# Performance work log

Hardware: AMD Instinct MI355X
Metric: run time of the kernel (lower is better)

Reference implementation:

```python
import jax, jax.numpy as jnp
import numpy as np

L, N, D, E, KD = 4, 40000, 128, 320000, 16
DECAY, N_ITER, EPS = 0.5, 3, 1e-5


def setup_inputs() -> dict:
    key = jax.random.key(0)
    ks = jax.random.split(key, 16)
    s = 0.05
    return {
        "x": jax.random.normal(ks[0], (L, N, D), jnp.float32),
        "edge_rows": jax.random.randint(ks[1], (E,), 0, N, jnp.int32),
        "edge_cols": jax.random.randint(ks[2], (E,), 0, N, jnp.int32),
        "edge_vals": jax.random.uniform(ks[3], (E,), jnp.float32) * 0.1,
        "sage_W": jax.random.normal(ks[4], (D, D), jnp.float32) * s,
        "sage_b": jnp.zeros((D,), jnp.float32),
        "sage_agg_W": jax.random.normal(ks[5], (D, D), jnp.float32) * s,
        "key_W": jax.random.normal(ks[6], (D, KD), jnp.float32) * s,
        "query_W": jax.random.normal(ks[7], (D, KD), jnp.float32) * s,
        "value_W": jax.random.normal(ks[8], (D, D), jnp.float32) * s,
        "attn_ln_g": jnp.ones((D,), jnp.float32),
        "attn_ln_b": jnp.zeros((D,), jnp.float32),
        "lin_W": jax.random.normal(ks[9], (D, D), jnp.float32) * s,
        "lin_b": jnp.zeros((D,), jnp.float32),
        "ln_g": jnp.ones((D,), jnp.float32),
        "ln_b": jnp.zeros((D,), jnp.float32),
    }


def _layernorm(x, g, b):
    mu = jnp.mean(x, axis=-1, keepdims=True)
    var = jnp.mean((x - mu) ** 2, axis=-1, keepdims=True)
    return (x - mu) * jax.lax.rsqrt(var + EPS) * g + b


def _spmm(rows, cols, vals, x2d):
    # sparse [N,N] @ dense [N,F]: out[r] = sum_e vals[e] * x2d[cols[e]] for rows[e]==r
    return jax.ops.segment_sum(vals[:, None] * x2d[cols], rows, num_segments=N)


def reference(x, edge_rows, edge_cols, edge_vals, sage_W, sage_b, sage_agg_W,
              key_W, query_W, value_W, attn_ln_g, attn_ln_b,
              lin_W, lin_b, ln_g, ln_b):
    # x: [L, N, D]
    x2d = jnp.transpose(x, (1, 0, 2)).reshape(N, L * D)  # [N, L*D]

    # ---- SAGEConv ----
    proj = x @ sage_W + sage_b
    agg = _spmm(edge_rows, edge_cols, edge_vals, x2d)
    agg = jnp.transpose(agg.reshape(N, L, D), (1, 0, 2)) @ sage_agg_W
    sage_out = jax.nn.silu(proj + agg)

    # ---- RetentiveAttention ----
    weights = jnp.mean((x @ key_W) * (x @ query_W), axis=-1, keepdims=True)
    x_acc = x
    cur = x2d
    for _ in range(1, N_ITER):
        cur = _spmm(edge_rows, edge_cols, edge_vals, cur * DECAY)
        xr = jnp.transpose(cur.reshape(N, L, D), (1, 0, 2))  # [L, N, D]
        weights = weights + jnp.mean((xr @ key_W) * (xr @ query_W), axis=-1, keepdims=True)
        x_acc = x_acc + xr
    attn_out = _layernorm((x_acc @ value_W) * weights, attn_ln_g, attn_ln_b)

    # ---- GPSConv fusion ----
    y = jax.nn.silu((sage_out + attn_out) @ lin_W + lin_b)
    return _layernorm(y, ln_g, ln_b)
```

## Files before the change

kernel.cpp:

```cpp
#include <hip/hip_runtime.h>
#include <math.h>

#define LL 4
#define NN 40000
#define DD 128
#define EE 320000
#define ROWS (LL*NN)
#define ND (NN*DD)
#define EPS_LN 1e-5f

typedef __attribute__((ext_vector_type(8))) short bf16x8;
typedef __attribute__((ext_vector_type(4))) short s16x4;
typedef __attribute__((ext_vector_type(4))) float f32x4;

#define OFF_CNT      0
#define OFF_ROWPTR   40000
#define OFF_ROWOFS   80004
#define OFF_CCOLS    120004
#define OFF_CVALS    440004
#define OFF_WBF      760004
#define OFF_A        829636
#define OFF_B        (OFF_A + ROWS*DD/2)
#define OFF_XBF      (OFF_B + ROWS*DD/2)

#define WB_W0  0
#define WB_W1  32768
#define WB_WV  65536
#define WB_WL  98304
#define WB_K   131072
#define WB_Q   135168
#define WB_LO_BIG 16384
#define WB_LO_KQ  2048
#define WB_LOGICAL 69632

__device__ __forceinline__ unsigned fu(float f) { union { float f; unsigned u; } v; v.f = f; return v.u; }
__device__ __forceinline__ float uf(unsigned u) { union { unsigned u; float f; } v; v.u = u; return v.f; }

__device__ __forceinline__ short f2bf(float f) {
    unsigned u = fu(f);
    unsigned r = u + 0x7fffu + ((u >> 16) & 1u);
    return (short)(r >> 16);
}
__device__ __forceinline__ float bf2f(short h) { return uf(((unsigned)(unsigned short)h) << 16); }
__device__ __forceinline__ void splitbf(float v, short& h, short& l) {
    h = f2bf(v);
    l = f2bf(v - bf2f(h));
}

__device__ __forceinline__ unsigned pack_hi(float a, float b) {
    return (fu(a) >> 16) | (fu(b) & 0xffff0000u);
}
__device__ __forceinline__ float resid(float a) {
    return a - uf(fu(a) & 0xffff0000u);
}

union FragU { bf16x8 v; unsigned u[4]; };

__global__ void k_hist(const int* __restrict__ rows, int* __restrict__ cnt) {
    int e = blockIdx.x * 256 + threadIdx.x;
    if (e < EE) atomicAdd(&cnt[rows[e]], 1);
}

__global__ __launch_bounds__(1024) void k_scan1(const int* __restrict__ cnt,
                                                int* __restrict__ row_ptr,
                                                int* __restrict__ bsum) {
    __shared__ int wtot[16];
    int tid = threadIdx.x, lane = tid & 63, wid = tid >> 6;
    int i = blockIdx.x * 1024 + tid;
    int v = (i < NN) ? cnt[i] : 0;
    int incl = v;
    #pragma unroll
    for (int off = 1; off < 64; off <<= 1) {
        int t = __shfl_up(incl, off);
        if (lane >= off) incl += t;
    }
    if (lane == 63) wtot[wid] = incl;
    __syncthreads();
    if (wid == 0) {
        int wv = (lane < 16) ? wtot[lane] : 0;
        #pragma unroll
        for (int off = 1; off < 16; off <<= 1) {
            int t = __shfl_up(wv, off);
            if (lane >= off) wv += t;
        }
        if (lane < 16) wtot[lane] = wv;
    }
    __syncthreads();
    int excl = ((wid > 0) ? wtot[wid - 1] : 0) + incl - v;
    if (i < NN) row_ptr[i] = excl;
    if (tid == 0) bsum[blockIdx.x] = wtot[15];
}

__global__ void k_scan2(const int* __restrict__ bsum, int* __restrict__ bofs) {
    int lane = threadIdx.x;
    int v = (lane < 40) ? bsum[lane] : 0;
    int incl = v;
    #pragma unroll
    for (int off = 1; off < 64; off <<= 1) {
        int t = __shfl_up(incl, off);
        if (lane >= off) incl += t;
    }
    if (lane < 40) bofs[lane] = incl - v;
    if (lane == 39) bofs[40] = incl;
}

__global__ __launch_bounds__(1024) void k_scan3(const int* __restrict__ bofs,
                                                int* __restrict__ row_ptr,
                                                int* __restrict__ row_ofs) {
    int i = blockIdx.x * 1024 + threadIdx.x;
    int add = bofs[blockIdx.x];
    if (i < NN) {
        int v = row_ptr[i] + add;
        row_ptr[i] = v;
        row_ofs[i] = v;
    }
    if (i == NN) row_ptr[NN] = bofs[40];
}

__global__ void k_scatter(const int* __restrict__ rows, const int* __restrict__ cols,
                          const float* __restrict__ vals, int* __restrict__ row_ofs,
                          int* __restrict__ csr_cols, float* __restrict__ csr_vals) {
    int e = blockIdx.x * 256 + threadIdx.x;
    if (e < EE) {
        int r = rows[e];
        int p = atomicAdd(&row_ofs[r], 1);
        csr_cols[p] = cols[e];
        csr_vals[p] = vals[e];
    }
}

__global__ __launch_bounds__(256) void k_xcast(const float* __restrict__ x, short* __restrict__ o) {
    size_t i = ((size_t)blockIdx.x * 256 + threadIdx.x) * 8;
    f32x4 a = *(const f32x4*)(x + i);
    f32x4 b = *(const f32x4*)(x + i + 4);
    bf16x8 r;
    #pragma unroll
    for (int j = 0; j < 4; ++j) { r[j] = f2bf(a[j]); r[j + 4] = f2bf(b[j]); }
    *(bf16x8*)(o + i) = r;
}

__global__ __launch_bounds__(64) void k_spmm(const short* __restrict__ in,
                                             const int* __restrict__ row_ptr,
                                             const int* __restrict__ ccols,
                                             const float* __restrict__ cvals,
                                             short* __restrict__ out) {
    int r = blockIdx.x;
    int lane = threadIdx.x;
    int l = lane >> 4;
    int c8 = (lane & 15) * 8;
    const short* inl = in + (size_t)l * ND + c8;
    float acc[8] = {0.f, 0.f, 0.f, 0.f, 0.f, 0.f, 0.f, 0.f};
    int e0 = row_ptr[r], e1 = row_ptr[r + 1];
    int e = e0;
    for (; e + 8 <= e1; e += 8) {
        int cc[8]; float vv[8]; bf16x8 xv[8];
        #pragma unroll
        for (int j = 0; j < 8; ++j) { cc[j] = ccols[e + j]; vv[j] = cvals[e + j]; }
        #pragma unroll
        for (int j = 0; j < 8; ++j) xv[j] = *(const bf16x8*)(inl + (size_t)cc[j] * DD);
        #pragma unroll
        for (int j = 0; j < 8; ++j)
            #pragma unroll
            for (int k = 0; k < 8; ++k) acc[k] += vv[j] * bf2f(xv[j][k]);
    }
    for (; e + 4 <= e1; e += 4) {
        int cc[4]; float vv[4]; bf16x8 xv[4];
        #pragma unroll
        for (int j = 0; j < 4; ++j) { cc[j] = ccols[e + j]; vv[j] = cvals[e + j]; }
        #pragma unroll
        for (int j = 0; j < 4; ++j) xv[j] = *(const bf16x8*)(inl + (size_t)cc[j] * DD);
        #pragma unroll
        for (int j = 0; j < 4; ++j)
            #pragma unroll
            for (int k = 0; k < 8; ++k) acc[k] += vv[j] * bf2f(xv[j][k]);
    }
    for (; e < e1; ++e) {
        int c = ccols[e];
        float v = cvals[e];
        bf16x8 xv = *(const bf16x8*)(inl + (size_t)c * DD);
        #pragma unroll
        for (int k = 0; k < 8; ++k) acc[k] += v * bf2f(xv[k]);
    }
    bf16x8 o;
    #pragma unroll
    for (int k = 0; k < 8; ++k) o[k] = f2bf(acc[k]);
    *(bf16x8*)(out + (size_t)l * ND + (size_t)r * DD + c8) = o;
}

__global__ void k_prep(const float* __restrict__ W0, const float* __restrict__ W1,
                       const float* __restrict__ Wv, const float* __restrict__ Wl,
                       const float* __restrict__ Kw, const float* __restrict__ Qw,
                       short* __restrict__ o) {
    int t = blockIdx.x * 256 + threadIdx.x;
    if (t >= WB_LOGICAL) return;
    float v;
    int hi_idx, lo_idx;
    if (t < 65536) {
        int m = t >> 14, idx = t & 16383;
        int nn = idx >> 7, kk = idx & 127;
        const float* M = (m == 0) ? W0 : (m == 1) ? W1 : (m == 2) ? Wv : Wl;
        v = M[kk * 128 + nn];
        hi_idx = m * 32768 + idx;
        lo_idx = hi_idx + WB_LO_BIG;
    } else {
        int t2 = t - 65536;
        int sel = t2 >> 11;
        int idx = t2 & 2047;
        int nn = idx >> 7, kk = idx & 127;
        const float* M = sel ? Qw : Kw;
        v = M[kk * 16 + nn];
        hi_idx = WB_K + sel * 4096 + idx;
        lo_idx = hi_idx + WB_LO_KQ;
    }
    short h, l;
    splitbf(v, h, l);
    o[hi_idx] = h;
    o[lo_idx] = l;
}

#define MFMA(a, b, c) __builtin_amdgcn_mfma_f32_16x16x32_bf16(a, b, c, 0, 0, 0)

__global__ __launch_bounds__(256, 4) void k_dense(
    const float* __restrict__ x, const short* __restrict__ A, const short* __restrict__ B,
    const short* __restrict__ wbf,
    const float* __restrict__ sage_b, const float* __restrict__ attn_g,
    const float* __restrict__ attn_b, const float* __restrict__ lin_b,
    const float* __restrict__ ln_g, const float* __restrict__ ln_b,
    float* __restrict__ out)
{
    __shared__ short pv[4][2][2048];
    const int tid = threadIdx.x;
    const int w = tid >> 6;
    const int lane = tid & 63;
    const int n = lane & 15;
    const int q = lane >> 4;
    const size_t rowA = (size_t)blockIdx.x * 64 + w * 16 + n;
    char* pB = (char*)&pv[w][0][0];
    char* vB = (char*)&pv[w][1][0];

    bf16x8 xh[4], ah[4], ch[4];
    f32x4 kx = {0,0,0,0}, qx = {0,0,0,0};
    f32x4 ka = {0,0,0,0}, qa = {0,0,0,0};
    f32x4 kb = {0,0,0,0}, qb = {0,0,0,0};

    {
        const float* xp = x + rowA * 128 + q * 8;
        const short* ap = A + rowA * 128 + q * 8;
        const short* bp = B + rowA * 128 + q * 8;
        const short* Kp = wbf + WB_K + n * 128 + q * 8;
        const short* Qp = wbf + WB_Q + n * 128 + q * 8;
        #pragma unroll
        for (int s = 0; s < 4; ++s) {
            f32x4 x0 = *(const f32x4*)(xp + s * 32);
            f32x4 x1 = *(const f32x4*)(xp + s * 32 + 4);
            bf16x8 av = *(const bf16x8*)(ap + s * 32);
            bf16x8 bv = *(const bf16x8*)(bp + s * 32);

            f32x4 c0, c1;
            #pragma unroll
            for (int j = 0; j < 4; ++j) {
                c0[j] = x0[j] + 0.5f * bf2f(av[j])     + 0.25f * bf2f(bv[j]);
                c1[j] = x1[j] + 0.5f * bf2f(av[j + 4]) + 0.25f * bf2f(bv[j + 4]);
            }

            FragU fxh, fxl, fch;
            #pragma unroll
            for (int i = 0; i < 2; ++i) {
                fxh.u[i]     = pack_hi(x0[2*i], x0[2*i+1]);
                fxh.u[i + 2] = pack_hi(x1[2*i], x1[2*i+1]);
                fxl.u[i]     = pack_hi(resid(x0[2*i]), resid(x0[2*i+1]));
                fxl.u[i + 2] = pack_hi(resid(x1[2*i]), resid(x1[2*i+1]));
                fch.u[i]     = pack_hi(c0[2*i], c0[2*i+1]);
                fch.u[i + 2] = pack_hi(c1[2*i], c1[2*i+1]);
            }
            xh[s] = fxh.v; ah[s] = av; ch[s] = fch.v;

            bf16x8 bkh = *(const bf16x8*)(Kp + s * 32);
            bf16x8 bkl = *(const bf16x8*)(Kp + WB_LO_KQ + s * 32);
            bf16x8 bqh = *(const bf16x8*)(Qp + s * 32);
            bf16x8 bql = *(const bf16x8*)(Qp + WB_LO_KQ + s * 32);
            kx = MFMA(fxh.v, bkh, kx); kx = MFMA(fxl.v, bkh, kx); kx = MFMA(fxh.v, bkl, kx);
            qx = MFMA(fxh.v, bqh, qx); qx = MFMA(fxl.v, bqh, qx); qx = MFMA(fxh.v, bql, qx);
            ka = MFMA(av, bkh, ka); qa = MFMA(av, bqh, qa);
            kb = MFMA(bv, bkh, kb); qb = MFMA(bv, bqh, qb);
        }
    }

    f32x4 wts;
    #pragma unroll
    for (int r = 0; r < 4; ++r) {
        float p = kx[r] * qx[r] + 0.25f * (ka[r] * qa[r]) + 0.0625f * (kb[r] * qb[r]);
        p += __shfl_xor(p, 1);
        p += __shfl_xor(p, 2);
        p += __shfl_xor(p, 4);
        p += __shfl_xor(p, 8);
        wts[r] = p * (1.f / 16.f);
    }

    {
        f32x4 S[8];
        #pragma unroll
        for (int t = 0; t < 8; ++t) {
            float bv = sage_b[t * 16 + n];
            S[t] = (f32x4){bv, bv, bv, bv};
        }
        #pragma unroll
        for (int s = 0; s < 4; ++s) {
            #pragma unroll
            for (int t = 0; t < 8; ++t) {
                bf16x8 w0h = *(const bf16x8*)(wbf + WB_W0 + (t * 16 + n) * 128 + s * 32 + q * 8);
                S[t] = MFMA(xh[s], w0h, S[t]);
                bf16x8 w1h = *(const bf16x8*)(wbf + WB_W1 + (t * 16 + n) * 128 + s * 32 + q * 8);
                S[t] = MFMA(ah[s], w1h, S[t]);
            }
        }
        #pragma unroll
        for (int t = 0; t < 8; ++t)
            #pragma unroll
            for (int r = 0; r < 4; ++r) {
                float v = S[t][r];
                v = v / (1.f + __expf(-v));
                int row = q * 4 + r;
                int byte = (row * 256 + (t * 16 + n) * 2) ^ ((row & 7) << 4);
                *(short*)(pB + byte) = f2bf(v);
            }
    }

    float mu_n, rs_n;
    {
        f32x4 V[8];
        #pragma unroll
        for (int t = 0; t < 8; ++t) V[t] = (f32x4){0.f, 0.f, 0.f, 0.f};
        #pragma unroll
        for (int s = 0; s < 4; ++s)
            #pragma unroll
            for (int t = 0; t < 8; ++t) {
                bf16x8 wvh = *(const bf16x8*)(wbf + WB_WV + (t * 16 + n) * 128 + s * 32 + q * 8);
                V[t] = MFMA(ch[s], wvh, V[t]);
            }
        f32x4 s1 = {0,0,0,0}, s2 = {0,0,0,0};
        #pragma unroll
        for (int t = 0; t < 8; ++t)
            #pragma unroll
            for (int r = 0; r < 4; ++r) {
                float v = V[t][r] * wts[r];
                V[t][r] = v;
                s1[r] += v; s2[r] += v * v;
            }
        #pragma unroll
        for (int r = 0; r < 4; ++r) {
            float a1 = s1[r], a2 = s2[r];
            a1 += __shfl_xor(a1, 1); a2 += __shfl_xor(a2, 1);
            a1 += __shfl_xor(a1, 2); a2 += __shfl_xor(a2, 2);
            a1 += __shfl_xor(a1, 4); a2 += __shfl_xor(a2, 4);
            a1 += __shfl_xor(a1, 8); a2 += __shfl_xor(a2, 8);
            s1[r] = a1; s2[r] = a2;
        }
        float mu4[4], rs4[4];
        #pragma unroll
        for (int r = 0; r < 4; ++r) {
            mu4[r] = s1[r] * (1.f / 128.f);
            float var = s2[r] * (1.f / 128.f) - mu4[r] * mu4[r];
            rs4[r] = rsqrtf(var + EPS_LN);
        }
        #pragma unroll
        for (int t = 0; t < 8; ++t)
            #pragma unroll
            for (int r = 0; r < 4; ++r) {
                int row = q * 4 + r;
                int byte = (row * 256 + (t * 16 + n) * 2) ^ ((row & 7) << 4);
                *(short*)(vB + byte) = f2bf(V[t][r]);
            }
        int src = (n >> 2) << 4;
        float mA = __shfl(mu4[0], src), mB_ = __shfl(mu4[1], src);
        float mC = __shfl(mu4[2], src), mD = __shfl(mu4[3], src);
        float rA = __shfl(rs4[0], src), rB_ = __shfl(rs4[1], src);
        float rC = __shfl(rs4[2], src), rD = __shfl(rs4[3], src);
        float m01 = (n & 1) ? mB_ : mA, m23 = (n & 1) ? mD : mC;
        float r01 = (n & 1) ? rB_ : rA, r23 = (n & 1) ? rD : rC;
        mu_n = (n & 2) ? m23 : m01;
        rs_n = (n & 2) ? r23 : r01;
    }

    bf16x8 zh[4];
    #pragma unroll
    for (int s = 0; s < 4; ++s) {
        int byte = (n * 256 + s * 64 + q * 16) ^ ((n & 7) << 4);
        bf16x8 ph = *(const bf16x8*)(pB + byte);
        bf16x8 vh = *(const bf16x8*)(vB + byte);
        const float* gp = attn_g + s * 32 + q * 8;
        const float* bp = attn_b + s * 32 + q * 8;
        f32x4 g0 = *(const f32x4*)gp, g1 = *(const f32x4*)(gp + 4);
        f32x4 b0 = *(const f32x4*)bp, b1 = *(const f32x4*)(bp + 4);
        float z[8];
        #pragma unroll
        for (int j = 0; j < 4; ++j) {
            z[j]     = bf2f(ph[j])     + (bf2f(vh[j])     - mu_n) * rs_n * g0[j] + b0[j];
            z[j + 4] = bf2f(ph[j + 4]) + (bf2f(vh[j + 4]) - mu_n) * rs_n * g1[j] + b1[j];
        }
        FragU f;
        f.u[0] = pack_hi(z[0], z[1]); f.u[1] = pack_hi(z[2], z[3]);
        f.u[2] = pack_hi(z[4], z[5]); f.u[3] = pack_hi(z[6], z[7]);
        zh[s] = f.v;
    }
    f32x4 F[8];
    #pragma unroll
    for (int t = 0; t < 8; ++t) {
        float bv = lin_b[t * 16 + n];
        F[t] = (f32x4){bv, bv, bv, bv};
    }
    #pragma unroll
    for (int s = 0; s < 4; ++s)
        #pragma unroll
        for (int t = 0; t < 8; ++t) {
            bf16x8 wlh = *(const bf16x8*)(wbf + WB_WL + (t * 16 + n) * 128 + s * 32 + q * 8);
            F[t] = MFMA(zh[s], wlh, F[t]);
        }
    f32x4 t1 = {0,0,0,0}, t2 = {0,0,0,0};
    #pragma unroll
    for (int t = 0; t < 8; ++t)
        #pragma unroll
        for (int r = 0; r < 4; ++r) {
            float v = F[t][r];
            v = v / (1.f + __expf(-v));
            F[t][r] = v;
            t1[r] += v; t2[r] += v * v;
        }
    #pragma unroll
    for (int r = 0; r < 4; ++r) {
        float a1 = t1[r], a2 = t2[r];
        a1 += __shfl_xor(a1, 1); a2 += __shfl_xor(a2, 1);
        a1 += __shfl_xor(a1, 2); a2 += __shfl_xor(a2, 2);
        a1 += __shfl_xor(a1, 4); a2 += __shfl_xor(a2, 4);
        a1 += __shfl_xor(a1, 8); a2 += __shfl_xor(a2, 8);
        t1[r] = a1; t2[r] = a2;
    }
    #pragma unroll
    for (int t = 0; t < 8; ++t) {
        float g = ln_g[t * 16 + n];
        float bb = ln_b[t * 16 + n];
        #pragma unroll
        for (int r = 0; r < 4; ++r) {
            float mu = t1[r] * (1.f / 128.f);
            float var = t2[r] * (1.f / 128.f) - mu * mu;
            float rs = rsqrtf(var + EPS_LN);
            size_t row = (size_t)blockIdx.x * 64 + w * 16 + q * 4 + r;
            out[row * 128 + t * 16 + n] = (F[t][r] - mu) * rs * g + bb;
        }
    }
}

extern "C" void kernel_launch(void* const* d_in, const int* in_sizes, int n_in,
                              void* d_out, int out_size, void* d_ws, size_t ws_size,
                              hipStream_t stream) {
    const float* x       = (const float*)d_in[0];
    const int*   erows   = (const int*)d_in[1];
    const int*   ecols   = (const int*)d_in[2];
    const float* evals   = (const float*)d_in[3];
    const float* sage_W  = (const float*)d_in[4];
    const float* sage_b  = (const float*)d_in[5];
    const float* sage_aW = (const float*)d_in[6];
    const float* key_W   = (const float*)d_in[7];
    const float* query_W = (const float*)d_in[8];
    const float* value_W = (const float*)d_in[9];
    const float* attn_g  = (const float*)d_in[10];
    const float* attn_b  = (const float*)d_in[11];
    const float* lin_W   = (const float*)d_in[12];
    const float* lin_b   = (const float*)d_in[13];
    const float* ln_g    = (const float*)d_in[14];
    const float* ln_b    = (const float*)d_in[15];
    float* out = (float*)d_out;

    int*   wsi = (int*)d_ws;
    float* wsf = (float*)d_ws;
    int*   cnt      = wsi + OFF_CNT;
    int*   row_ptr  = wsi + OFF_ROWPTR;
    int*   row_ofs  = wsi + OFF_ROWOFS;
    int*   csr_cols = wsi + OFF_CCOLS;
    float* csr_vals = wsf + OFF_CVALS;
    short* wbf      = (short*)(wsf + OFF_WBF);
    short* Abf      = (short*)(wsf + OFF_A);
    short* Bbf      = (short*)(wsf + OFF_B);
    short* Xbf      = (short*)(wsf + OFF_XBF);
    int*   bsum     = (int*)(wsf + OFF_A);
    int*   bofs     = bsum + 64;

    hipMemsetAsync(cnt, 0, NN * sizeof(int), stream);
    k_hist<<<(EE + 255) / 256, 256, 0, stream>>>(erows, cnt);
    k_prep<<<(WB_LOGICAL + 255) / 256, 256, 0, stream>>>(sage_W, sage_aW, value_W, lin_W,
                                                         key_W, query_W, wbf);
    k_xcast<<<ROWS * DD / (256 * 8), 256, 0, stream>>>(x, Xbf);
    k_scan1<<<40, 1024, 0, stream>>>(cnt, row_ptr, bsum);
    k_scan2<<<1, 64, 0, stream>>>(bsum, bofs);
    k_scan3<<<40, 1024, 0, stream>>>(bofs, row_ptr, row_ofs);
    k_scatter<<<(EE + 255) / 256, 256, 0, stream>>>(erows, ecols, evals, row_ofs, csr_cols, csr_vals);

    k_spmm<<<NN, 64, 0, stream>>>(Xbf, row_ptr, csr_cols, csr_vals, Abf);
    k_spmm<<<NN, 64, 0, stream>>>(Abf, row_ptr, csr_cols, csr_vals, Bbf);

    k_dense<<<ROWS / 64, 256, 0, stream>>>(x, Abf, Bbf, wbf, sage_b, attn_g, attn_b,
                                           lin_b, ln_g, ln_b, out);
}
```

Baseline: 597.8 us.

## Store bf16 node features node-major to gather contiguous rows in SpMM

Changes the bf16 feature buffers from [L,N,D] to a node-major [N,L*D] layout. Each SpMM gather then reads one contiguous 1KB row per edge instead of four 256B pieces, and SpMM blocks now hold four rows of 64 threads each. The dense kernel indexes the new layout and moves the combined-input fragments into LDS to cut register pressure, dropping the occupancy hint in launch_bounds. Fewer blocks and the wider gathers aim to improve memory efficiency, at the cost of extra LDS traffic in the dense kernel.

```diff
diff --git a/kernel.cpp b/kernel.cpp
--- a/kernel.cpp
+++ b/kernel.cpp
@@ -130,25 +130,29 @@
 }
 
 __global__ __launch_bounds__(256) void k_xcast(const float* __restrict__ x, short* __restrict__ o) {
-    size_t i = ((size_t)blockIdx.x * 256 + threadIdx.x) * 8;
-    f32x4 a = *(const f32x4*)(x + i);
-    f32x4 b = *(const f32x4*)(x + i + 4);
-    bf16x8 r;
-    #pragma unroll
-    for (int j = 0; j < 4; ++j) { r[j] = f2bf(a[j]); r[j + 4] = f2bf(b[j]); }
-    *(bf16x8*)(o + i) = r;
-}
-
-__global__ __launch_bounds__(64) void k_spmm(const short* __restrict__ in,
-                                             const int* __restrict__ row_ptr,
-                                             const int* __restrict__ ccols,
-                                             const float* __restrict__ cvals,
-                                             short* __restrict__ out) {
-    int r = blockIdx.x;
-    int lane = threadIdx.x;
-    int l = lane >> 4;
-    int c8 = (lane & 15) * 8;
-    const short* inl = in + (size_t)l * ND + c8;
+    int t = blockIdx.x * 256 + threadIdx.x;
+    int n = t >> 4;
+    int d8 = (t & 15) * 8;
+    #pragma unroll
+    for (int l = 0; l < LL; ++l) {
+        const float* xp = x + (size_t)l * ND + (size_t)n * 128 + d8;
+        f32x4 a = *(const f32x4*)xp;
+        f32x4 b = *(const f32x4*)(xp + 4);
+        bf16x8 r;
+        #pragma unroll
+        for (int j = 0; j < 4; ++j) { r[j] = f2bf(a[j]); r[j + 4] = f2bf(b[j]); }
+        *(bf16x8*)(o + (size_t)n * 512 + l * 128 + d8) = r;
+    }
+}
+
+__global__ __launch_bounds__(256) void k_spmm(const short* __restrict__ in,
+                                              const int* __restrict__ row_ptr,
+                                              const int* __restrict__ ccols,
+                                              const float* __restrict__ cvals,
+                                              short* __restrict__ out) {
+    int r = blockIdx.x * 4 + (threadIdx.x >> 6);
+    int lane = threadIdx.x & 63;
+    const short* inl = in + lane * 8;
     float acc[8] = {0.f, 0.f, 0.f, 0.f, 0.f, 0.f, 0.f, 0.f};
     int e0 = row_ptr[r], e1 = row_ptr[r + 1];
     int e = e0;
@@ -157,7 +161,7 @@
         #pragma unroll
         for (int j = 0; j < 8; ++j) { cc[j] = ccols[e + j]; vv[j] = cvals[e + j]; }
         #pragma unroll
-        for (int j = 0; j < 8; ++j) xv[j] = *(const bf16x8*)(inl + (size_t)cc[j] * DD);
+        for (int j = 0; j < 8; ++j) xv[j] = *(const bf16x8*)(inl + (size_t)cc[j] * 512);
         #pragma unroll
         for (int j = 0; j < 8; ++j)
             #pragma unroll
@@ -168,7 +172,7 @@
         #pragma unroll
         for (int j = 0; j < 4; ++j) { cc[j] = ccols[e + j]; vv[j] = cvals[e + j]; }
         #pragma unroll
-        for (int j = 0; j < 4; ++j) xv[j] = *(const bf16x8*)(inl + (size_t)cc[j] * DD);
+        for (int j = 0; j < 4; ++j) xv[j] = *(const bf16x8*)(inl + (size_t)cc[j] * 512);
         #pragma unroll
         for (int j = 0; j < 4; ++j)
             #pragma unroll
@@ -177,14 +181,14 @@
     for (; e < e1; ++e) {
         int c = ccols[e];
         float v = cvals[e];
-        bf16x8 xv = *(const bf16x8*)(inl + (size_t)c * DD);
+        bf16x8 xv = *(const bf16x8*)(inl + (size_t)c * 512);
         #pragma unroll
         for (int k = 0; k < 8; ++k) acc[k] += v * bf2f(xv[k]);
     }
     bf16x8 o;
     #pragma unroll
     for (int k = 0; k < 8; ++k) o[k] = f2bf(acc[k]);
-    *(bf16x8*)(out + (size_t)l * ND + (size_t)r * DD + c8) = o;
+    *(bf16x8*)(out + (size_t)r * 512 + lane * 8) = o;
 }
 
 __global__ void k_prep(const float* __restrict__ W0, const float* __restrict__ W1,
@@ -220,7 +224,7 @@
 
 #define MFMA(a, b, c) __builtin_amdgcn_mfma_f32_16x16x32_bf16(a, b, c, 0, 0, 0)
 
-__global__ __launch_bounds__(256, 4) void k_dense(
+__global__ __launch_bounds__(256) void k_dense(
     const float* __restrict__ x, const short* __restrict__ A, const short* __restrict__ B,
     const short* __restrict__ wbf,
     const float* __restrict__ sage_b, const float* __restrict__ attn_g,
@@ -234,19 +238,21 @@
     const int lane = tid & 63;
     const int n = lane & 15;
     const int q = lane >> 4;
-    const size_t rowA = (size_t)blockIdx.x * 64 + w * 16 + n;
+    const int rowA = blockIdx.x * 64 + w * 16 + n;
+    const int l = rowA / NN;
+    const int node = rowA - l * NN;
     char* pB = (char*)&pv[w][0][0];
     char* vB = (char*)&pv[w][1][0];
 
-    bf16x8 xh[4], ah[4], ch[4];
+    bf16x8 xh[4], ah[4];
     f32x4 kx = {0,0,0,0}, qx = {0,0,0,0};
     f32x4 ka = {0,0,0,0}, qa = {0,0,0,0};
     f32x4 kb = {0,0,0,0}, qb = {0,0,0,0};
 
     {
-        const float* xp = x + rowA * 128 + q * 8;
-        const short* ap = A + rowA * 128 + q * 8;
-        const short* bp = B + rowA * 128 + q * 8;
+        const float* xp = x + (size_t)rowA * 128 + q * 8;
+        const short* ap = A + (size_t)node * 512 + l * 128 + q * 8;
+        const short* bp = B + (size_t)node * 512 + l * 128 + q * 8;
         const short* Kp = wbf + WB_K + n * 128 + q * 8;
         const short* Qp = wbf + WB_Q + n * 128 + q * 8;
         #pragma unroll
@@ -273,7 +279,9 @@
                 fch.u[i]     = pack_hi(c0[2*i], c0[2*i+1]);
                 fch.u[i + 2] = pack_hi(c1[2*i], c1[2*i+1]);
             }
-            xh[s] = fxh.v; ah[s] = av; ch[s] = fch.v;
+            xh[s] = fxh.v; ah[s] = av;
+            int cbyte = (n * 256 + s * 64 + q * 16) ^ ((n & 7) << 4);
+            *(bf16x8*)(vB + cbyte) = fch.v;
 
             bf16x8 bkh = *(const bf16x8*)(Kp + s * 32);
             bf16x8 bkl = *(const bf16x8*)(Kp + WB_LO_KQ + s * 32);
@@ -285,6 +293,7 @@
             kb = MFMA(bv, bkh, kb); qb = MFMA(bv, bqh, qb);
         }
     }
+    asm volatile("" ::: "memory");
 
     f32x4 wts;
     #pragma unroll
@@ -325,6 +334,7 @@
                 *(short*)(pB + byte) = f2bf(v);
             }
     }
+    asm volatile("" ::: "memory");
 
     float mu_n, rs_n;
     {
@@ -332,12 +342,15 @@
         #pragma unroll
         for (int t = 0; t < 8; ++t) V[t] = (f32x4){0.f, 0.f, 0.f, 0.f};
         #pragma unroll
-        for (int s = 0; s < 4; ++s)
+        for (int s = 0; s < 4; ++s) {
+            int cbyte = (n * 256 + s * 64 + q * 16) ^ ((n & 7) << 4);
+            bf16x8 chs = *(const bf16x8*)(vB + cbyte);
             #pragma unroll
             for (int t = 0; t < 8; ++t) {
                 bf16x8 wvh = *(const bf16x8*)(wbf + WB_WV + (t * 16 + n) * 128 + s * 32 + q * 8);
-                V[t] = MFMA(ch[s], wvh, V[t]);
-            }
+                V[t] = MFMA(chs, wvh, V[t]);
+            }
+        }
         f32x4 s1 = {0,0,0,0}, s2 = {0,0,0,0};
         #pragma unroll
         for (int t = 0; t < 8; ++t)
@@ -381,6 +394,7 @@
         mu_n = (n & 2) ? m23 : m01;
         rs_n = (n & 2) ? r23 : r01;
     }
+    asm volatile("" ::: "memory");
 
     bf16x8 zh[4];
     #pragma unroll
@@ -489,14 +503,14 @@
     k_hist<<<(EE + 255) / 256, 256, 0, stream>>>(erows, cnt);
     k_prep<<<(WB_LOGICAL + 255) / 256, 256, 0, stream>>>(sage_W, sage_aW, value_W, lin_W,
                                                          key_W, query_W, wbf);
-    k_xcast<<<ROWS * DD / (256 * 8), 256, 0, stream>>>(x, Xbf);
+    k_xcast<<<NN * 16 / 256, 256, 0, stream>>>(x, Xbf);
     k_scan1<<<40, 1024, 0, stream>>>(cnt, row_ptr, bsum);
     k_scan2<<<1, 64, 0, stream>>>(bsum, bofs);
     k_scan3<<<40, 1024, 0, stream>>>(bofs, row_ptr, row_ofs);
     k_scatter<<<(EE + 255) / 256, 256, 0, stream>>>(erows, ecols, evals, row_ofs, csr_cols, csr_vals);
 
-    k_spmm<<<NN, 64, 0, stream>>>(Xbf, row_ptr, csr_cols, csr_vals, Abf);
-    k_spmm<<<NN, 64, 0, stream>>>(Abf, row_ptr, csr_cols, csr_vals, Bbf);
+    k_spmm<<<NN / 4, 256, 0, stream>>>(Xbf, row_ptr, csr_cols, csr_vals, Abf);
+    k_spmm<<<NN / 4, 256, 0, stream>>>(Abf, row_ptr, csr_cols, csr_vals, Bbf);
 
     k_dense<<<ROWS / 64, 256, 0, stream>>>(x, Abf, Bbf, wbf, sage_b, attn_g, attn_b,
                                            lin_b, ln_g, ln_b, out);
```

New measurement: 530.0 us. -11.3%, faster.
